# Kernel optimization log

Hardware: AMD Instinct MI355X
Metric: run time of the kernel (lower is better)

Reference implementation:

```python
import jax, jax.numpy as jnp
import numpy as np

N = 100000
E = 1600000
IN_C = 256
HID = 64
OUT_C = 64
HEADS = 2
NEG_SLOPE = 0.2


def setup_inputs() -> dict:
    key = jax.random.key(0)
    ks = jax.random.split(key, 12)
    x = jax.random.normal(ks[0], (N, IN_C), dtype=jnp.float32)
    edge_index = jax.random.randint(ks[1], (2, E), 0, N, dtype=jnp.int64)
    s = 0.1
    # GATConv 1: in=IN_C, out=HID, heads=HEADS, concat=True
    W1 = jax.random.normal(ks[2], (IN_C, HEADS * HID), dtype=jnp.float32) * s
    a_src1 = jax.random.normal(ks[3], (HEADS, HID), dtype=jnp.float32) * s
    a_dst1 = jax.random.normal(ks[4], (HEADS, HID), dtype=jnp.float32) * s
    b1 = jnp.zeros((HEADS * HID,), dtype=jnp.float32)
    # GATConv 2: in=HEADS*HID, out=OUT_C, heads=1, concat=False
    W2 = jax.random.normal(ks[5], (HEADS * HID, OUT_C), dtype=jnp.float32) * s
    a_src2 = jax.random.normal(ks[6], (1, OUT_C), dtype=jnp.float32) * s
    a_dst2 = jax.random.normal(ks[7], (1, OUT_C), dtype=jnp.float32) * s
    b2 = jnp.zeros((OUT_C,), dtype=jnp.float32)
    # MLP head: Linear(OUT_C, HID), Linear(HID, OUT_C)
    W_lin1 = jax.random.normal(ks[8], (OUT_C, HID), dtype=jnp.float32) * s
    b_lin1 = jnp.zeros((HID,), dtype=jnp.float32)
    W_lin2 = jax.random.normal(ks[9], (HID, OUT_C), dtype=jnp.float32) * s
    b_lin2 = jnp.zeros((OUT_C,), dtype=jnp.float32)
    return {"x": x, "edge_index": edge_index,
            "W1": W1, "a_src1": a_src1, "a_dst1": a_dst1, "b1": b1,
            "W2": W2, "a_src2": a_src2, "a_dst2": a_dst2, "b2": b2,
            "W_lin1": W_lin1, "b_lin1": b_lin1,
            "W_lin2": W_lin2, "b_lin2": b_lin2}


def gat_conv(x, src, dst, W, a_src, a_dst, b, concat):
    # src/dst already include self loops (PyG add_self_loops=True default)
    n = x.shape[0]
    H, C = a_src.shape
    h = (x @ W).reshape(n, H, C)                      # [N,H,C]
    alpha_src = (h * a_src).sum(-1)                   # [N,H]
    alpha_dst = (h * a_dst).sum(-1)                   # [N,H]
    e = jax.nn.leaky_relu(alpha_src[src] + alpha_dst[dst], NEG_SLOPE)  # [E',H]
    # segment softmax over destination node
    m = jax.ops.segment_max(e, dst, num_segments=n)
    e = jnp.exp(e - m[dst])
    denom = jax.ops.segment_sum(e, dst, num_segments=n)
    alpha = e / (denom[dst] + 1e-16)                  # [E',H]
    msg = alpha[:, :, None] * h[src]                  # [E',H,C]
    out = jax.ops.segment_sum(msg, dst, num_segments=n)  # [N,H,C]
    out = out.reshape(n, H * C) if concat else out.mean(axis=1)
    return out + b


def reference(x, edge_index, W1, a_src1, a_dst1, b1, W2, a_src2, a_dst2, b2,
              W_lin1, b_lin1, W_lin2, b_lin2):
    n = x.shape[0]
    loop = jnp.arange(n, dtype=edge_index.dtype)
    src = jnp.concatenate([edge_index[0], loop])
    dst = jnp.concatenate([edge_index[1], loop])
    h = jax.nn.elu(gat_conv(x, src, dst, W1, a_src1, a_dst1, b1, concat=True))
    h = gat_conv(h, src, dst, W2, a_src2, a_dst2, b2, concat=False)
    # dropout is identity in eval mode
    h = jax.nn.elu(h @ W_lin1 + b_lin1)
    h = h @ W_lin2 + b_lin2
    # batch = zeros -> single graph; global_mean_pool = mean over nodes
    return h.mean(axis=0, keepdims=True)              # [1, OUT_C]
```

## Files before the change

kernel.cpp:

```cpp
#include <hip/hip_runtime.h>
#include <hip/hip_bf16.h>

constexpr int NN = 100000;
constexpr int NE = 1600000;
constexpr int EP = NE + NN;
constexpr float NEG = 0.2f;

__device__ __forceinline__ float elu_f(float x) { return x > 0.f ? x : __expf(x) - 1.f; }

__device__ __forceinline__ void f4fma(float4& a, float s, const float4& b) {
    a.x += s * b.x; a.y += s * b.y; a.z += s * b.z; a.w += s * b.w;
}

__device__ __forceinline__ unsigned short bf16rne(float f) {
    unsigned int u = __float_as_uint(f);
    u += 0x7fffu + ((u >> 16) & 1u);
    return (unsigned short)(u >> 16);
}
__device__ __forceinline__ unsigned int pk2(float lo, float hi) {
    return (unsigned int)bf16rne(lo) | ((unsigned int)bf16rne(hi) << 16);
}

template<int K, int M, int BN>
__global__ __launch_bounds__(256) void gemm_tiled(const float* __restrict__ X,
                                                  const float* __restrict__ W,
                                                  float* __restrict__ H,
                                                  unsigned short* __restrict__ Hb) {
    constexpr int KT = 32;
    constexpr int CG = M / 8;
    constexpr int NG = 256 / CG;
    static_assert(NG * 8 == BN, "BN must equal 8*256/CG");
    __shared__ float Xs[KT * BN];
    __shared__ float Ws[KT * M];
    int tid = threadIdx.x;
    int cg = tid % CG, ng = tid / CG;
    int n0 = ng * 8, c0 = cg * 8;
    int nodeBase = blockIdx.x * BN;

    float4 acc[8][2];
#pragma unroll
    for (int i = 0; i < 8; ++i) {
        acc[i][0] = make_float4(0.f, 0.f, 0.f, 0.f);
        acc[i][1] = make_float4(0.f, 0.f, 0.f, 0.f);
    }

    for (int k0 = 0; k0 < K; k0 += KT) {
#pragma unroll
        for (int r = 0; r < BN / 32; ++r) {
            int ln = tid / 8 + 32 * r;
            int kk = (tid % 8) * 4;
            int node = nodeBase + ln;
            node = node < NN ? node : NN - 1;
            float4 v = *reinterpret_cast<const float4*>(X + (size_t)node * K + k0 + kk);
            Xs[(kk + 0) * BN + ln] = v.x;
            Xs[(kk + 1) * BN + ln] = v.y;
            Xs[(kk + 2) * BN + ln] = v.z;
            Xs[(kk + 3) * BN + ln] = v.w;
        }
#pragma unroll
        for (int r = 0; r < (KT * M) / 1024; ++r) {
            int f = tid + 256 * r;
            *reinterpret_cast<float4*>(Ws + 4 * f) =
                *reinterpret_cast<const float4*>(W + (size_t)k0 * M + 4 * f);
        }
        __syncthreads();
#pragma unroll
        for (int k = 0; k < KT; ++k) {
            const float4 xa = *reinterpret_cast<const float4*>(Xs + k * BN + n0);
            const float4 xb = *reinterpret_cast<const float4*>(Xs + k * BN + n0 + 4);
            const float4 wa = *reinterpret_cast<const float4*>(Ws + k * M + c0);
            const float4 wb = *reinterpret_cast<const float4*>(Ws + k * M + c0 + 4);
            f4fma(acc[0][0], xa.x, wa); f4fma(acc[0][1], xa.x, wb);
            f4fma(acc[1][0], xa.y, wa); f4fma(acc[1][1], xa.y, wb);
            f4fma(acc[2][0], xa.z, wa); f4fma(acc[2][1], xa.z, wb);
            f4fma(acc[3][0], xa.w, wa); f4fma(acc[3][1], xa.w, wb);
            f4fma(acc[4][0], xb.x, wa); f4fma(acc[4][1], xb.x, wb);
            f4fma(acc[5][0], xb.y, wa); f4fma(acc[5][1], xb.y, wb);
            f4fma(acc[6][0], xb.z, wa); f4fma(acc[6][1], xb.z, wb);
            f4fma(acc[7][0], xb.w, wa); f4fma(acc[7][1], xb.w, wb);
        }
        __syncthreads();
    }
#pragma unroll
    for (int i = 0; i < 8; ++i) {
        int node = nodeBase + n0 + i;
        if (node < NN) {
            *reinterpret_cast<float4*>(H + (size_t)node * M + c0)     = acc[i][0];
            *reinterpret_cast<float4*>(H + (size_t)node * M + c0 + 4) = acc[i][1];
            uint4 p;
            p.x = pk2(acc[i][0].x, acc[i][0].y);
            p.y = pk2(acc[i][0].z, acc[i][0].w);
            p.z = pk2(acc[i][1].x, acc[i][1].y);
            p.w = pk2(acc[i][1].z, acc[i][1].w);
            *reinterpret_cast<uint4*>(Hb + (size_t)node * M + c0) = p;
        }
    }
}

template<int H, int C>
__global__ void alpha_kernel(const float* __restrict__ Hm, const float* __restrict__ a_src,
                             const float* __restrict__ a_dst,
                             float* __restrict__ as, float* __restrict__ ad) {
    int idx = blockIdx.x * blockDim.x + threadIdx.x;
    if (idx >= NN * H) return;
    int node = idx / H, h = idx % H;
    const float* hr = Hm + (size_t)node * (H * C) + h * C;
    const float* sr = a_src + h * C;
    const float* dr = a_dst + h * C;
    float s = 0.f, d = 0.f;
#pragma unroll
    for (int c = 0; c < C; c += 4) {
        float4 hv = *reinterpret_cast<const float4*>(hr + c);
        float4 sv = *reinterpret_cast<const float4*>(sr + c);
        float4 dv = *reinterpret_cast<const float4*>(dr + c);
        s += hv.x * sv.x + hv.y * sv.y + hv.z * sv.z + hv.w * sv.w;
        d += hv.x * dv.x + hv.y * dv.y + hv.z * dv.z + hv.w * dv.w;
    }
    as[idx] = s; ad[idx] = d;
}

__global__ void count_deg_kernel(const int* __restrict__ ei, int* __restrict__ deg) {
    int i = blockIdx.x * blockDim.x + threadIdx.x;
    if (i >= EP) return;
    int d = (i < NE) ? ei[NE + i] : (i - NE);
    atomicAdd(&deg[d], 1);
}

__global__ __launch_bounds__(256) void scan1_kernel(const int* __restrict__ deg,
                                                    int* __restrict__ excl,
                                                    int* __restrict__ partials) {
    __shared__ int ts[256];
    int tid = threadIdx.x;
    int idx0 = blockIdx.x * 1024 + tid * 4;
    int v0 = (idx0 + 0 < NN) ? deg[idx0 + 0] : 0;
    int v1 = (idx0 + 1 < NN) ? deg[idx0 + 1] : 0;
    int v2 = (idx0 + 2 < NN) ? deg[idx0 + 2] : 0;
    int v3 = (idx0 + 3 < NN) ? deg[idx0 + 3] : 0;
    int s0 = v0, s1 = s0 + v1, s2 = s1 + v2, s3 = s2 + v3;
    ts[tid] = s3;
    __syncthreads();
    for (int off = 1; off < 256; off <<= 1) {
        int t = (tid >= off) ? ts[tid - off] : 0;
        __syncthreads();
        ts[tid] += t;
        __syncthreads();
    }
    int te = ts[tid] - s3;
    if (idx0 + 0 < NN) excl[idx0 + 0] = te;
    if (idx0 + 1 < NN) excl[idx0 + 1] = te + s0;
    if (idx0 + 2 < NN) excl[idx0 + 2] = te + s1;
    if (idx0 + 3 < NN) excl[idx0 + 3] = te + s2;
    if (tid == 255) partials[blockIdx.x] = ts[255];
}

__global__ void scan2_kernel(int* __restrict__ partials, int nb) {
    if (threadIdx.x == 0 && blockIdx.x == 0) {
        int run = 0;
        for (int i = 0; i < nb; ++i) { int t = partials[i]; partials[i] = run; run += t; }
    }
}

__global__ void scan3_kernel(int* __restrict__ row_ptr, int* __restrict__ cursor,
                             const int* __restrict__ partials) {
    int i = blockIdx.x * blockDim.x + threadIdx.x;
    if (i == 0) row_ptr[NN] = EP;
    if (i >= NN) return;
    int v = row_ptr[i] + partials[i >> 10];
    row_ptr[i] = v;
    cursor[i] = v;
}

__global__ void scatter_kernel(const int* __restrict__ ei, int* __restrict__ cursor,
                               int* __restrict__ csr_src) {
    int i = blockIdx.x * blockDim.x + threadIdx.x;
    if (i >= EP) return;
    int s, d;
    if (i < NE) { s = ei[i]; d = ei[NE + i]; }
    else        { s = d = i - NE; }
    int pos = atomicAdd(&cursor[d], 1);
    csr_src[pos] = s;
}

__global__ __launch_bounds__(256) void agg1_kernel(const int* __restrict__ rp,
                                                   const int* __restrict__ cs,
                                                   const unsigned short* __restrict__ h1b,
                                                   const float* __restrict__ as,
                                                   const float* __restrict__ ad,
                                                   const float* __restrict__ b,
                                                   float* __restrict__ out1) {
    int wid = threadIdx.x >> 6, lane = threadIdx.x & 63;
    int node = blockIdx.x * 4 + wid;
    if (node >= NN) return;
    int h = lane >> 5;
    int c0 = 2 * lane;
    float adv = ad[2 * node + h];
    float accx = 0.f, accy = 0.f, wsum = 0.f;
    int beg = rp[node], end = rp[node + 1];

    int sA = cs[beg];
    int sB = (beg + 1 < end) ? cs[beg + 1] : 0;
    float2 asA = *reinterpret_cast<const float2*>(as + 2 * sA);
    unsigned int pA = *reinterpret_cast<const unsigned int*>(h1b + (size_t)sA * 128 + c0);
    for (int j = beg; j < end; ++j) {
        int sC = (j + 2 < end) ? cs[j + 2] : 0;
        float2 asB = *reinterpret_cast<const float2*>(as + 2 * sB);
        unsigned int pB = *reinterpret_cast<const unsigned int*>(h1b + (size_t)sB * 128 + c0);
        float e = (h ? asA.y : asA.x) + adv;
        e = e > 0.f ? e : NEG * e;
        float w = __expf(e);
        float hx = __uint_as_float(pA << 16);
        float hy = __uint_as_float(pA & 0xffff0000u);
        accx += w * hx; accy += w * hy; wsum += w;
        asA = asB; pA = pB; sB = sC;
    }
    float inv = 1.f / (wsum + 1e-16f);
    float2 o;
    o.x = elu_f(accx * inv + b[c0 + 0]);
    o.y = elu_f(accy * inv + b[c0 + 1]);
    *reinterpret_cast<float2*>(out1 + (size_t)node * 128 + c0) = o;
}

__global__ __launch_bounds__(256) void agg2_kernel(const int* __restrict__ rp,
                                                   const int* __restrict__ cs,
                                                   const unsigned short* __restrict__ h2b,
                                                   const float* __restrict__ as,
                                                   const float* __restrict__ ad,
                                                   const float* __restrict__ b2,
                                                   float* __restrict__ out2) {
    int wid = threadIdx.x >> 6, lane = threadIdx.x & 63;
    int node = blockIdx.x * 4 + wid;
    if (node >= NN) return;
    float adv = ad[node];
    float acc = 0.f, wsum = 0.f;
    int beg = rp[node], end = rp[node + 1];

    int sA = cs[beg];
    int sB = (beg + 1 < end) ? cs[beg + 1] : 0;
    float asA = as[sA];
    unsigned short pA = h2b[(size_t)sA * 64 + lane];
    for (int j = beg; j < end; ++j) {
        int sC = (j + 2 < end) ? cs[j + 2] : 0;
        float asB = as[sB];
        unsigned short pB = h2b[(size_t)sB * 64 + lane];
        float e = asA + adv;
        e = e > 0.f ? e : NEG * e;
        float w = __expf(e);
        float hv = __uint_as_float(((unsigned int)pA) << 16);
        acc += w * hv; wsum += w;
        asA = asB; pA = pB; sB = sC;
    }
    out2[(size_t)node * 64 + lane] = acc / (wsum + 1e-16f) + b2[lane];
}

__global__ __launch_bounds__(256) void mlp_pool_kernel(const float* __restrict__ out2,
                                                       const float* __restrict__ Wl1,
                                                       const float* __restrict__ bl1,
                                                       const float* __restrict__ Wl2,
                                                       const float* __restrict__ bl2,
                                                       float* __restrict__ pool) {
    __shared__ float sW1[64 * 64];
    __shared__ float sW2[64 * 64];
    __shared__ float sv[4][64];
    __shared__ float st[4][64];
    __shared__ float sacc[256];
    int tid = threadIdx.x;
    for (int i = tid; i < 64 * 64; i += 256) { sW1[i] = Wl1[i]; sW2[i] = Wl2[i]; }
    __syncthreads();
    int ln = tid / 64, c = tid % 64;
    float bl1c = bl1[c], bl2c = bl2[c];
    float acc = 0.f;
    for (int base = blockIdx.x * 4; base < NN; base += gridDim.x * 4) {
        int node = base + ln;
        float v = 0.f;
        if (node < NN) v = out2[(size_t)node * 64 + c];
        sv[ln][c] = v;
        __syncthreads();
        float t = bl1c;
#pragma unroll
        for (int k = 0; k < 64; ++k) t += sv[ln][k] * sW1[k * 64 + c];
        t = t > 0.f ? t : __expf(t) - 1.f;
        st[ln][c] = t;
        __syncthreads();
        float o = bl2c;
#pragma unroll
        for (int k = 0; k < 64; ++k) o += st[ln][k] * sW2[k * 64 + c];
        if (node < NN) acc += o;
        __syncthreads();
    }
    sacc[tid] = acc;
    __syncthreads();
    if (tid < 64) {
        float r = sacc[tid] + sacc[64 + tid] + sacc[128 + tid] + sacc[192 + tid];
        atomicAdd(&pool[tid], r);
    }
}

__global__ void finalize_kernel(const float* __restrict__ pool, float* __restrict__ out) {
    int c = threadIdx.x;
    if (c < 64) out[c] = pool[c] * (1.0f / NN);
}

extern "C" void kernel_launch(void* const* d_in, const int* in_sizes, int n_in,
                              void* d_out, int out_size, void* d_ws, size_t ws_size,
                              hipStream_t stream) {
    const float* x      = (const float*)d_in[0];
    const int*   ei     = (const int*)d_in[1];
    const float* W1     = (const float*)d_in[2];
    const float* a_src1 = (const float*)d_in[3];
    const float* a_dst1 = (const float*)d_in[4];
    const float* b1     = (const float*)d_in[5];
    const float* W2     = (const float*)d_in[6];
    const float* a_src2 = (const float*)d_in[7];
    const float* a_dst2 = (const float*)d_in[8];
    const float* b2     = (const float*)d_in[9];
    const float* Wl1    = (const float*)d_in[10];
    const float* bl1    = (const float*)d_in[11];
    const float* Wl2    = (const float*)d_in[12];
    const float* bl2    = (const float*)d_in[13];
    float* out = (float*)d_out;

    float* ws = (float*)d_ws;
    size_t o = 0;
    float* h1      = ws + o; o += (size_t)NN * 128;
    float* out1    = ws + o; o += (size_t)NN * 128;
    float* h2      = ws + o; o += (size_t)NN * 64;
    float* as1     = ws + o; o += NN * 2;
    float* ad1     = ws + o; o += NN * 2;
    float* as2     = ws + o; o += NN;
    float* ad2     = ws + o; o += NN;
    float* pool    = ws + o; o += 64;
    int* deg       = (int*)(ws + o); o += NN;
    int* row_ptr   = (int*)(ws + o); o += NN + 2;
    int* cursor    = (int*)(ws + o); o += NN;
    int* partials  = (int*)(ws + o); o += 128;
    int* csr_src   = (int*)(ws + o); o += EP;

    unsigned short* h1b = (unsigned short*)h2;
    float* out2         = h1;
    unsigned short* h2b = (unsigned short*)(h1 + (size_t)NN * 64);

    constexpr int SCAN_BLOCKS = (NN + 1023) / 1024;

    hipMemsetAsync(deg, 0, (size_t)NN * sizeof(int), stream);
    hipMemsetAsync(pool, 0, 64 * sizeof(float), stream);
    count_deg_kernel<<<(EP + 255) / 256, 256, 0, stream>>>(ei, deg);
    scan1_kernel<<<SCAN_BLOCKS, 256, 0, stream>>>(deg, row_ptr, partials);
    scan2_kernel<<<1, 64, 0, stream>>>(partials, SCAN_BLOCKS);
    scan3_kernel<<<(NN + 255) / 256, 256, 0, stream>>>(row_ptr, cursor, partials);
    scatter_kernel<<<(EP + 255) / 256, 256, 0, stream>>>(ei, cursor, csr_src);

    gemm_tiled<256, 128, 128><<<(NN + 127) / 128, 256, 0, stream>>>(x, W1, h1, h1b);
    alpha_kernel<2, 64><<<(NN * 2 + 255) / 256, 256, 0, stream>>>(h1, a_src1, a_dst1, as1, ad1);
    agg1_kernel<<<(NN + 3) / 4, 256, 0, stream>>>(row_ptr, csr_src, h1b, as1, ad1, b1, out1);

    gemm_tiled<128, 64, 256><<<(NN + 255) / 256, 256, 0, stream>>>(out1, W2, h2, h2b);
    alpha_kernel<1, 64><<<(NN + 255) / 256, 256, 0, stream>>>(h2, a_src2, a_dst2, as2, ad2);
    agg2_kernel<<<(NN + 3) / 4, 256, 0, stream>>>(row_ptr, csr_src, h2b, as2, ad2, b2, out2);

    mlp_pool_kernel<<<2048, 256, 0, stream>>>(out2, Wl1, bl1, Wl2, bl2, pool);
    finalize_kernel<<<1, 64, 0, stream>>>(pool, out);
}
```

Measured before the change: 826.9 us.

## Record per-edge rank during degree count to remove scatter atomics

The degree-count pass now keeps the return value of its atomicAdd as each edge's rank within its destination bucket. The scatter pass then writes csr_src[row_ptr[d]+rank[i]] directly, with no second atomicAdd on a cursor array. Both edge kernels also process four edges per thread so several loads and atomics are in flight at once. The cost is an extra EP-sized rank array that is written once and read once.

```diff
diff --git a/kernel.cpp b/kernel.cpp
--- a/kernel.cpp
+++ b/kernel.cpp
@@ -5,6 +5,7 @@
 constexpr int NE = 1600000;
 constexpr int EP = NE + NN;
 constexpr float NEG = 0.2f;
+constexpr int EPT = 4;
 
 __device__ __forceinline__ float elu_f(float x) { return x > 0.f ? x : __expf(x) - 1.f; }
 
@@ -119,11 +120,27 @@
     as[idx] = s; ad[idx] = d;
 }
 
-__global__ void count_deg_kernel(const int* __restrict__ ei, int* __restrict__ deg) {
-    int i = blockIdx.x * blockDim.x + threadIdx.x;
-    if (i >= EP) return;
-    int d = (i < NE) ? ei[NE + i] : (i - NE);
-    atomicAdd(&deg[d], 1);
+__global__ __launch_bounds__(256) void count_rank_kernel(const int* __restrict__ ei,
+                                                         int* __restrict__ deg,
+                                                         int* __restrict__ rank) {
+    int base = blockIdx.x * (256 * EPT) + threadIdx.x;
+    int d[EPT];
+#pragma unroll
+    for (int e = 0; e < EPT; ++e) {
+        int i = base + e * 256;
+        if (i < EP) d[e] = (i < NE) ? ei[NE + i] : (i - NE);
+    }
+    int pos[EPT];
+#pragma unroll
+    for (int e = 0; e < EPT; ++e) {
+        int i = base + e * 256;
+        if (i < EP) pos[e] = atomicAdd(&deg[d[e]], 1);
+    }
+#pragma unroll
+    for (int e = 0; e < EPT; ++e) {
+        int i = base + e * 256;
+        if (i < EP) rank[i] = pos[e];
+    }
 }
 
 __global__ __launch_bounds__(256) void scan1_kernel(const int* __restrict__ deg,
@@ -160,25 +177,27 @@
     }
 }
 
-__global__ void scan3_kernel(int* __restrict__ row_ptr, int* __restrict__ cursor,
-                             const int* __restrict__ partials) {
+__global__ void scan3_kernel(int* __restrict__ row_ptr, const int* __restrict__ partials) {
     int i = blockIdx.x * blockDim.x + threadIdx.x;
     if (i == 0) row_ptr[NN] = EP;
     if (i >= NN) return;
-    int v = row_ptr[i] + partials[i >> 10];
-    row_ptr[i] = v;
-    cursor[i] = v;
-}
-
-__global__ void scatter_kernel(const int* __restrict__ ei, int* __restrict__ cursor,
-                               int* __restrict__ csr_src) {
-    int i = blockIdx.x * blockDim.x + threadIdx.x;
-    if (i >= EP) return;
-    int s, d;
-    if (i < NE) { s = ei[i]; d = ei[NE + i]; }
-    else        { s = d = i - NE; }
-    int pos = atomicAdd(&cursor[d], 1);
-    csr_src[pos] = s;
+    row_ptr[i] += partials[i >> 10];
+}
+
+__global__ __launch_bounds__(256) void scatter2_kernel(const int* __restrict__ ei,
+                                                       const int* __restrict__ rank,
+                                                       const int* __restrict__ row_ptr,
+                                                       int* __restrict__ csr_src) {
+    int base = blockIdx.x * (256 * EPT) + threadIdx.x;
+#pragma unroll
+    for (int e = 0; e < EPT; ++e) {
+        int i = base + e * 256;
+        if (i >= EP) continue;
+        int s, d;
+        if (i < NE) { s = ei[i]; d = ei[NE + i]; }
+        else        { s = d = i - NE; }
+        csr_src[row_ptr[d] + rank[i]] = s;
+    }
 }
 
 __global__ __launch_bounds__(256) void agg1_kernel(const int* __restrict__ rp,
@@ -331,7 +350,7 @@
     float* pool    = ws + o; o += 64;
     int* deg       = (int*)(ws + o); o += NN;
     int* row_ptr   = (int*)(ws + o); o += NN + 2;
-    int* cursor    = (int*)(ws + o); o += NN;
+    int* rank      = (int*)(ws + o); o += EP;
     int* partials  = (int*)(ws + o); o += 128;
     int* csr_src   = (int*)(ws + o); o += EP;
 
@@ -340,14 +359,15 @@
     unsigned short* h2b = (unsigned short*)(h1 + (size_t)NN * 64);
 
     constexpr int SCAN_BLOCKS = (NN + 1023) / 1024;
+    constexpr int EDGE_BLOCKS = (EP + 256 * EPT - 1) / (256 * EPT);
 
     hipMemsetAsync(deg, 0, (size_t)NN * sizeof(int), stream);
     hipMemsetAsync(pool, 0, 64 * sizeof(float), stream);
-    count_deg_kernel<<<(EP + 255) / 256, 256, 0, stream>>>(ei, deg);
+    count_rank_kernel<<<EDGE_BLOCKS, 256, 0, stream>>>(ei, deg, rank);
     scan1_kernel<<<SCAN_BLOCKS, 256, 0, stream>>>(deg, row_ptr, partials);
     scan2_kernel<<<1, 64, 0, stream>>>(partials, SCAN_BLOCKS);
-    scan3_kernel<<<(NN + 255) / 256, 256, 0, stream>>>(row_ptr, cursor, partials);
-    scatter_kernel<<<(EP + 255) / 256, 256, 0, stream>>>(ei, cursor, csr_src);
+    scan3_kernel<<<(NN + 255) / 256, 256, 0, stream>>>(row_ptr, partials);
+    scatter2_kernel<<<EDGE_BLOCKS, 256, 0, stream>>>(ei, rank, row_ptr, csr_src);
 
     gemm_tiled<256, 128, 128><<<(NN + 127) / 128, 256, 0, stream>>>(x, W1, h1, h1b);
     alpha_kernel<2, 64><<<(NN * 2 + 255) / 256, 256, 0, stream>>>(h1, a_src1, a_dst1, as1, ad1);
```

Result: faster. 748.3 us (-9.5%).
